# Performance work log

Hardware: AMD Instinct MI355X
Metric: run time of the kernel (lower is better)

Reference implementation:

```python
import jax, jax.numpy as jnp
import numpy as np

EPS = 1e-5

def _layernorm(x, g, b):
    mu = jnp.mean(x, axis=-1, keepdims=True)
    var = jnp.mean(jnp.square(x - mu), axis=-1, keepdims=True)
    return (x - mu) * jax.lax.rsqrt(var + EPS) * g + b

def _mlp(x, w1, b1, w2, b2):
    h = jax.nn.gelu(jnp.einsum('bnd,dh->bnh', x, w1) + b1, approximate=False)
    return jnp.einsum('bnh,hd->bnd', h, w2) + b2

def setup_inputs() -> dict:
    key = jax.random.key(0)
    B, N, D, H = 2, 8192, 1024, 4096
    ks = jax.random.split(key, 12)
    s1 = 1.0 / np.sqrt(D)
    s2 = 1.0 / np.sqrt(H)
    return {
        'x': jax.random.normal(ks[0], (B, N, D), dtype=jnp.float32),
        'mask': jax.random.randint(ks[1], (B, N), 0, 2) > 0,
        'g_rgb': jnp.ones((D,), jnp.float32),
        'b_rgb': jnp.zeros((D,), jnp.float32),
        'w1_rgb': jax.random.normal(ks[2], (D, H), dtype=jnp.float32) * s1,
        'b1_rgb': jnp.zeros((H,), jnp.float32),
        'w2_rgb': jax.random.normal(ks[3], (H, D), dtype=jnp.float32) * s2,
        'b2_rgb': jnp.zeros((D,), jnp.float32),
        'g_expr': jnp.ones((D,), jnp.float32),
        'b_expr': jnp.zeros((D,), jnp.float32),
        'w1_expr': jax.random.normal(ks[4], (D, H), dtype=jnp.float32) * s1,
        'b1_expr': jnp.zeros((H,), jnp.float32),
        'w2_expr': jax.random.normal(ks[5], (H, D), dtype=jnp.float32) * s2,
        'b2_expr': jnp.zeros((D,), jnp.float32),
    }

def reference(x, mask, g_rgb, b_rgb, w1_rgb, b1_rgb, w2_rgb, b2_rgb,
              g_expr, b_expr, w1_expr, b1_expr, w2_expr, b2_expr):
    # Per-token routing: rgb expert where mask, expr expert where ~mask.
    # LayerNorm+MLP are pointwise per token, so dense compute + select is
    # mathematically identical to the torch gather->compute->scatter.
    z_rgb = _mlp(_layernorm(x, g_rgb, b_rgb), w1_rgb, b1_rgb, w2_rgb, b2_rgb)
    z_expr = _mlp(_layernorm(x, g_expr, b_expr), w1_expr, b1_expr, w2_expr, b2_expr)
    z = jnp.where(mask[..., None], z_rgb, z_expr)
    return z.astype(jnp.float16)  # torch scatters into a float16 buffer
```

## Files before the change

kernel.cpp:

```cpp
#include <hip/hip_runtime.h>
#include <hip/hip_bf16.h>
#include <hip/hip_fp16.h>

#define D_ 1024
#define H_ 4096
#define NTOK 16384
#define MPAD 16640

typedef __attribute__((ext_vector_type(8))) short bf16x8;
typedef __attribute__((ext_vector_type(4))) float f32x4;

static __device__ __forceinline__ unsigned short f2bf(float f) {
  union { float f; unsigned u; } x; x.f = f;
  unsigned u = x.u + 0x7fffu + ((x.u >> 16) & 1u);
  return (unsigned short)(u >> 16);
}

static __device__ __forceinline__ void gld16(const void* g, void* l) {
  __builtin_amdgcn_global_load_lds(
      (const __attribute__((address_space(1))) unsigned int*)g,
      (__attribute__((address_space(3))) unsigned int*)l, 16, 0, 0);
}

static __device__ __forceinline__ float gelu_fast(float x) {
  const float z = x * (1.5957691216f + 0.0713548163f * x * x);
  return x * __builtin_amdgcn_rcpf(1.0f + __expf(-z));
}

__global__ __launch_bounds__(256) void transpose4_kernel(
    const float* __restrict__ w1r, const float* __restrict__ w1e,
    const float* __restrict__ w2r, const float* __restrict__ w2e,
    unsigned short* __restrict__ o1r, unsigned short* __restrict__ o1e,
    unsigned short* __restrict__ o2r, unsigned short* __restrict__ o2e,
    const int* __restrict__ mask, int* __restrict__ perm, int* __restrict__ counts) {
  __shared__ union SMem {
    float tile[64][65];
    struct { int sm[NTOK]; int wsum[4]; } c;
  } u;
  const int t = blockIdx.x;
  if (t == 4096) {
    const int NT = 256, CH = NTOK / NT;
    const int tt = threadIdx.x;
    const int ln = tt & 63, wv = tt >> 6;
    for (int i = tt; i < NTOK; i += NT) u.c.sm[i] = mask[i];
    for (int i = tt; i < MPAD; i += NT) perm[i] = -1;
    __syncthreads();
    const int base = tt * CH;
    int cnt = 0;
    for (int i = 0; i < CH; ++i) cnt += (u.c.sm[base + i] != 0);
    int sc = cnt;
#pragma unroll
    for (int o = 1; o < 64; o <<= 1) {
      int up = __shfl_up(sc, o, 64);
      if (ln >= o) sc += up;
    }
    if (ln == 63) u.c.wsum[wv] = sc;
    __syncthreads();
    int woff = 0;
#pragma unroll
    for (int j = 0; j < 4; ++j) woff += (j < wv) ? u.c.wsum[j] : 0;
    const int total1 = u.c.wsum[0] + u.c.wsum[1] + u.c.wsum[2] + u.c.wsum[3];
    if (tt == 0) { counts[0] = total1; counts[1] = NTOK - total1; }
    const int excl = woff + sc - cnt;
    const int expr_base = ((total1 + 255) >> 8) << 8;
    int p1 = excl;
    int p0 = expr_base + (base - excl);
    for (int i = 0; i < CH; ++i) {
      const int idx = base + i;
      if (u.c.sm[idx] != 0) perm[p1++] = idx; else perm[p0++] = idx;
    }
    return;
  }
  const float* src; unsigned short* dst; int R, C, tl;
  if (t < 1024)       { src = w1r; dst = o1r; R = D_; C = H_; tl = t; }
  else if (t < 2048)  { src = w1e; dst = o1e; R = D_; C = H_; tl = t - 1024; }
  else if (t < 3072)  { src = w2r; dst = o2r; R = H_; C = D_; tl = t - 2048; }
  else                { src = w2e; dst = o2e; R = H_; C = D_; tl = t - 3072; }
  const int tc = C >> 6;
  const int r0 = (tl / tc) * 64, c0 = (tl % tc) * 64;
  const int tx = threadIdx.x & 63, ty = threadIdx.x >> 6;
#pragma unroll
  for (int i = 0; i < 64; i += 4)
    u.tile[ty + i][tx] = src[(size_t)(r0 + ty + i) * C + c0 + tx];
  __syncthreads();
  const int wl = threadIdx.x & 31, wrow = threadIdx.x >> 5;
#pragma unroll
  for (int i = 0; i < 64; i += 8) {
    const int orow = wrow + i;
    const unsigned lo = f2bf(u.tile[2 * wl][orow]);
    const unsigned hi = f2bf(u.tile[2 * wl + 1][orow]);
    *(unsigned*)(dst + (size_t)(c0 + orow) * R + r0 + 2 * wl) = lo | (hi << 16);
  }
}

__global__ __launch_bounds__(512) void ln_kernel(
    const float* __restrict__ x, const int* __restrict__ mask,
    const int* __restrict__ perm,
    const float* __restrict__ g_rgb, const float* __restrict__ b_rgb,
    const float* __restrict__ g_expr, const float* __restrict__ b_expr,
    unsigned short* __restrict__ xln) {
  const int h = threadIdx.x >> 8;
  const int tid = threadIdx.x & 255;
  const int i = blockIdx.x * 2 + h;
  int t = perm[i];
  const bool live = t >= 0;
  if (!live) t = 0;
  const float4 v = ((const float4*)(x + (size_t)t * D_))[tid];
  float s = v.x + v.y + v.z + v.w;
  float ss = v.x * v.x + v.y * v.y + v.z * v.z + v.w * v.w;
#pragma unroll
  for (int o = 32; o > 0; o >>= 1) {
    s += __shfl_xor(s, o, 64);
    ss += __shfl_xor(ss, o, 64);
  }
  __shared__ float red[16];
  const int wv = threadIdx.x >> 6, ln = threadIdx.x & 63;
  if (ln == 0) { red[wv] = s; red[8 + wv] = ss; }
  __syncthreads();
  const int rb = h * 4;
  s = red[rb + 0] + red[rb + 1] + red[rb + 2] + red[rb + 3];
  ss = red[8 + rb + 0] + red[8 + rb + 1] + red[8 + rb + 2] + red[8 + rb + 3];
  const float mu = s * (1.0f / D_);
  const float var = ss * (1.0f / D_) - mu * mu;
  const float rs = rsqrtf(var + 1e-5f);
  const bool rgb = mask[t] != 0;
  const float4 gv = ((const float4*)(rgb ? g_rgb : g_expr))[tid];
  const float4 bv = ((const float4*)(rgb ? b_rgb : b_expr))[tid];
  const unsigned short o0 = f2bf((v.x - mu) * rs * gv.x + bv.x);
  const unsigned short o1 = f2bf((v.y - mu) * rs * gv.y + bv.y);
  const unsigned short o2 = f2bf((v.z - mu) * rs * gv.z + bv.z);
  const unsigned short o3 = f2bf((v.w - mu) * rs * gv.w + bv.w);
  uint2 pk;
  pk.x = (unsigned)o0 | ((unsigned)o1 << 16);
  pk.y = (unsigned)o2 | ((unsigned)o3 << 16);
  if (live) *((uint2*)(xln + (size_t)i * D_ + tid * 4)) = pk;
}

template <int K, int N>
__global__ __launch_bounds__(512, 2) void gemm8_kernel(
    const unsigned short* __restrict__ A,
    const unsigned short* __restrict__ Wt_rgb,
    const unsigned short* __restrict__ Wt_expr,
    const float* __restrict__ bias_rgb,
    const float* __restrict__ bias_expr,
    const int* __restrict__ counts,
    unsigned short* __restrict__ Out) {
  constexpr int MT = MPAD / 256;
  constexpr int NT = N / 256;
  constexpr int ntk = K / 64;
  constexpr int KH2 = 128 * K * 2;

  const int tid = threadIdx.x;
  const int id = blockIdx.x;
  const int xcd = id & 7;
  const int slot = id >> 3;
  const int p = xcd * ((MT * NT) / 8) + slot;
  const int m0 = (p / NT) * 256;
  const int n0 = (p % NT) * 256;
  const int cnt_rgb = counts[0];
  const unsigned short* Wt = (m0 < cnt_rgb) ? Wt_rgb : Wt_expr;
  const float* bias = (m0 < cnt_rgb) ? bias_rgb : bias_expr;

  __shared__ unsigned short As[2][256 * 64];
  __shared__ unsigned short Bs[2][256 * 64];

  const int lane = tid & 63, wave = tid >> 6;
  const int wr = wave >> 2, wc = wave & 3;
  const int quad = lane >> 4, l16 = lane & 15;

  f32x4 acc[8][4] = {};

  const char* Abase = (const char*)A;
  const char* Wbase = (const char*)Wt;

  int agK0, agK1, bgK0, bgK1, sl0, sl1;
  {
    const int s0 = tid, s1 = 512 + tid;
    const int r0 = s0 >> 3, r1 = s1 >> 3;
    const int ks0 = ((s0 ^ r0) & 7) * 8, ks1 = ((s1 ^ r1) & 7) * 8;
    agK0 = ((m0 + r0) * K + ks0) * 2;  agK1 = ((m0 + r1) * K + ks1) * 2;
    bgK0 = ((n0 + r0) * K + ks0) * 2;  bgK1 = ((n0 + r1) * K + ks1) * 2;
    sl0 = s0 * 16;  sl1 = s1 * 16;
  }

  int aoffL[2][2][4];
  int boffL[2][4];
#pragma unroll
  for (int kk = 0; kk < 2; ++kk) {
    const int cb = kk * 4 + quad;
#pragma unroll
    for (int mh = 0; mh < 2; ++mh)
#pragma unroll
      for (int mi = 0; mi < 4; ++mi) {
        const int row = wr * 128 + mh * 64 + mi * 16 + l16;
        aoffL[kk][mh][mi] = (row * 64 + ((cb ^ row) & 7) * 8) * 2;
      }
#pragma unroll
    for (int ni = 0; ni < 4; ++ni) {
      const int row = wc * 64 + ni * 16 + l16;
      boffL[kk][ni] = (row * 64 + ((cb ^ row) & 7) * 8) * 2;
    }
  }

  bf16x8 a0, a1, a2, a3;
  bf16x8 bb[4];

#define STAGE_A(T1, HA, Q) do { \
    gld16(Abase + agK0 + (HA) * KH2 + (T1) * 128, (char*)As + (Q) * 32768 + (HA) * 16384 + sl0); \
    gld16(Abase + agK1 + (HA) * KH2 + (T1) * 128, (char*)As + (Q) * 32768 + (HA) * 16384 + sl1); \
  } while (0)
#define STAGE_B(T2, HB, Q) do { \
    gld16(Wbase + bgK0 + (HB) * KH2 + (T2) * 128, (char*)Bs + (Q) * 32768 + (HB) * 16384 + sl0); \
    gld16(Wbase + bgK1 + (HB) * KH2 + (T2) * 128, (char*)Bs + (Q) * 32768 + (HB) * 16384 + sl1); \
  } while (0)
#define RD_A(P_, KK, MH) do { \
    const char* _ab = (const char*)As + (P_) * 32768; \
    a0 = *(const bf16x8*)(_ab + aoffL[KK][MH][0]); \
    a1 = *(const bf16x8*)(_ab + aoffL[KK][MH][1]); \
    a2 = *(const bf16x8*)(_ab + aoffL[KK][MH][2]); \
    a3 = *(const bf16x8*)(_ab + aoffL[KK][MH][3]); \
  } while (0)
#define RD_B(P_, KK) do { \
    const char* _bp = (const char*)Bs + (P_) * 32768; \
    bb[0] = *(const bf16x8*)(_bp + boffL[KK][0]); \
    bb[1] = *(const bf16x8*)(_bp + boffL[KK][1]); \
    bb[2] = *(const bf16x8*)(_bp + boffL[KK][2]); \
    bb[3] = *(const bf16x8*)(_bp + boffL[KK][3]); \
  } while (0)
#define MFMA16(MO) do { \
    acc[(MO)+0][0] = __builtin_amdgcn_mfma_f32_16x16x32_bf16(a0, bb[0], acc[(MO)+0][0], 0, 0, 0); \
    acc[(MO)+0][1] = __builtin_amdgcn_mfma_f32_16x16x32_bf16(a0, bb[1], acc[(MO)+0][1], 0, 0, 0); \
    acc[(MO)+0][2] = __builtin_amdgcn_mfma_f32_16x16x32_bf16(a0, bb[2], acc[(MO)+0][2], 0, 0, 0); \
    acc[(MO)+0][3] = __builtin_amdgcn_mfma_f32_16x16x32_bf16(a0, bb[3], acc[(MO)+0][3], 0, 0, 0); \
    acc[(MO)+1][0] = __builtin_amdgcn_mfma_f32_16x16x32_bf16(a1, bb[0], acc[(MO)+1][0], 0, 0, 0); \
    acc[(MO)+1][1] = __builtin_amdgcn_mfma_f32_16x16x32_bf16(a1, bb[1], acc[(MO)+1][1], 0, 0, 0); \
    acc[(MO)+1][2] = __builtin_amdgcn_mfma_f32_16x16x32_bf16(a1, bb[2], acc[(MO)+1][2], 0, 0, 0); \
    acc[(MO)+1][3] = __builtin_amdgcn_mfma_f32_16x16x32_bf16(a1, bb[3], acc[(MO)+1][3], 0, 0, 0); \
    acc[(MO)+2][0] = __builtin_amdgcn_mfma_f32_16x16x32_bf16(a2, bb[0], acc[(MO)+2][0], 0, 0, 0); \
    acc[(MO)+2][1] = __builtin_amdgcn_mfma_f32_16x16x32_bf16(a2, bb[1], acc[(MO)+2][1], 0, 0, 0); \
    acc[(MO)+2][2] = __builtin_amdgcn_mfma_f32_16x16x32_bf16(a2, bb[2], acc[(MO)+2][2], 0, 0, 0); \
    acc[(MO)+2][3] = __builtin_amdgcn_mfma_f32_16x16x32_bf16(a2, bb[3], acc[(MO)+2][3], 0, 0, 0); \
    acc[(MO)+3][0] = __builtin_amdgcn_mfma_f32_16x16x32_bf16(a3, bb[0], acc[(MO)+3][0], 0, 0, 0); \
    acc[(MO)+3][1] = __builtin_amdgcn_mfma_f32_16x16x32_bf16(a3, bb[1], acc[(MO)+3][1], 0, 0, 0); \
    acc[(MO)+3][2] = __builtin_amdgcn_mfma_f32_16x16x32_bf16(a3, bb[2], acc[(MO)+3][2], 0, 0, 0); \
    acc[(MO)+3][3] = __builtin_amdgcn_mfma_f32_16x16x32_bf16(a3, bb[3], acc[(MO)+3][3], 0, 0, 0); \
  } while (0)

#define KTILE(T_, P_, SA_, SB_, VMC_) do { \
     \
    RD_B(P_, 0); RD_A(P_, 0, 0); \
    if (SA_) STAGE_A((T_) + 1, 0, (P_) ^ 1); \
    __builtin_amdgcn_s_barrier(); \
    __builtin_amdgcn_s_setprio(1); MFMA16(0); __builtin_amdgcn_s_setprio(0); \
    __builtin_amdgcn_s_barrier(); \
     \
    RD_A(P_, 0, 1); \
    if (SA_) STAGE_A((T_) + 1, 1, (P_) ^ 1); \
    __builtin_amdgcn_s_barrier(); \
    __builtin_amdgcn_s_setprio(1); MFMA16(4); __builtin_amdgcn_s_setprio(0); \
    __builtin_amdgcn_s_barrier(); \
     \
    RD_B(P_, 1); RD_A(P_, 1, 0); \
    __builtin_amdgcn_s_barrier(); \
    __builtin_amdgcn_s_setprio(1); MFMA16(0); __builtin_amdgcn_s_setprio(0); \
    __builtin_amdgcn_s_barrier(); \
     \
    RD_A(P_, 1, 1); \
    if (SB_) { STAGE_B((T_) + 2, 0, P_); STAGE_B((T_) + 2, 1, P_); } \
    __builtin_amdgcn_s_barrier(); \
    __builtin_amdgcn_s_setprio(1); MFMA16(4); __builtin_amdgcn_s_setprio(0); \
    if ((VMC_) == 4) { asm volatile("s_waitcnt vmcnt(4)" ::: "memory"); } \
    else if ((VMC_) == 0) { asm volatile("s_waitcnt vmcnt(0)" ::: "memory"); } \
    __builtin_amdgcn_sched_barrier(0); \
    __builtin_amdgcn_s_barrier(); \
  } while (0)

  STAGE_A(0, 0, 0); STAGE_A(0, 1, 0);
  STAGE_B(0, 0, 0); STAGE_B(0, 1, 0);
  STAGE_B(1, 0, 1); STAGE_B(1, 1, 1);
  asm volatile("s_waitcnt vmcnt(4)" ::: "memory");
  __builtin_amdgcn_sched_barrier(0);
  __builtin_amdgcn_s_barrier();

  for (int tt = 0; tt < ntk / 2 - 1; ++tt) {
    const int t0 = tt * 2;
    KTILE(t0, 0, 1, 1, 4);
    KTILE(t0 + 1, 1, 1, 1, 4);
  }
  KTILE(ntk - 2, 0, 1, 0, 0);
  KTILE(ntk - 1, 1, 0, 0, -1);

#undef KTILE
#undef MFMA16
#undef RD_B
#undef RD_A
#undef STAGE_B
#undef STAGE_A

  float bv[4];
#pragma unroll
  for (int ni = 0; ni < 4; ++ni) bv[ni] = bias[n0 + wc * 64 + ni * 16 + l16];
#pragma unroll
  for (int mi = 0; mi < 8; ++mi) {
#pragma unroll
    for (int r = 0; r < 4; ++r) {
      const int row = m0 + wr * 128 + mi * 16 + quad * 4 + r;
      unsigned short* orow = Out + (size_t)row * N + n0 + wc * 64 + l16;
#pragma unroll
      for (int ni = 0; ni < 4; ++ni)
        orow[ni * 16] = f2bf(gelu_fast(acc[mi][ni][r] + bv[ni]));
    }
  }
}

template <int EP, int K, int N>
__global__ __launch_bounds__(256) void gemm_kernel(
    const unsigned short* __restrict__ A,
    const unsigned short* __restrict__ Wt_rgb,
    const unsigned short* __restrict__ Wt_expr,
    const float* __restrict__ bias_rgb,
    const float* __restrict__ bias_expr,
    const int* __restrict__ counts,
    const int* __restrict__ perm,
    void* __restrict__ OutP,
    const int mbase) {
  constexpr int BM = 128, BN = 128, BK = 64;
  constexpr int MTH = (MPAD / 2) / BM;
  constexpr int NT = N / BN;
  const int tid = threadIdx.x;
  const int id = blockIdx.x;
  const int xcd = id & 7;
  const int slot = id >> 3;
  const int p = xcd * ((MTH * NT) / 8) + slot;
  const int m0 = mbase + (p / NT) * BM;
  const int n0 = (p % NT) * BN;
  const int cnt_rgb = counts[0];
  const unsigned short* Wt = (m0 < cnt_rgb) ? Wt_rgb : Wt_expr;
  const float* bias = (m0 < cnt_rgb) ? bias_rgb : bias_expr;

  __shared__ unsigned short As[BM * BK];
  __shared__ unsigned short Bs[BN * BK];

  f32x4 acc[4][4] = {};

  const int lane = tid & 63, wave = tid >> 6;
  const int wm = (wave & 1) * 64, wn = (wave >> 1) * 64;
  const int quad = lane >> 4, l16 = lane & 15;

  const char* Abase = (const char*)A;
  const char* Wbase = (const char*)Wt;
  const char* AsB = (const char*)As;
  const char* BsB = (const char*)Bs;

  int ag[4], bg[4], sl[4];
#pragma unroll
  for (int it = 0; it < 4; ++it) {
    const int s = it * 256 + tid;
    const int row = s >> 3;
    const int ks = ((s ^ row) & 7) * 8;
    ag[it] = ((m0 + row) * K + ks) * 2;
    bg[it] = ((n0 + row) * K + ks) * 2;
    sl[it] = s * 16;
  }
  int aoff[2][4], boff[2][4];
#pragma unroll
  for (int hh = 0; hh < 2; ++hh) {
    const int cb = hh * 4 + quad;
#pragma unroll
    for (int mi = 0; mi < 4; ++mi) {
      const int row = wm + mi * 16 + l16;
      aoff[hh][mi] = (row * BK + (((cb ^ row) & 7) << 3)) * 2;
    }
#pragma unroll
    for (int ni = 0; ni < 4; ++ni) {
      const int row = wn + ni * 16 + l16;
      boff[hh][ni] = (row * BK + (((cb ^ row) & 7) << 3)) * 2;
    }
  }

  for (int k0 = 0; k0 < K; k0 += BK) {
#pragma unroll
    for (int it = 0; it < 4; ++it) {
      gld16(Abase + ag[it], (void*)(AsB + sl[it]));
      gld16(Wbase + bg[it], (void*)(BsB + sl[it]));
      ag[it] += BK * 2;
      bg[it] += BK * 2;
    }
    __syncthreads();
#pragma unroll
    for (int hh = 0; hh < 2; ++hh) {
      bf16x8 a[4], b[4];
#pragma unroll
      for (int mi = 0; mi < 4; ++mi) a[mi] = *(const bf16x8*)(AsB + aoff[hh][mi]);
#pragma unroll
      for (int ni = 0; ni < 4; ++ni) b[ni] = *(const bf16x8*)(BsB + boff[hh][ni]);
#pragma unroll
      for (int mi = 0; mi < 4; ++mi)
#pragma unroll
        for (int ni = 0; ni < 4; ++ni)
          acc[mi][ni] = __builtin_amdgcn_mfma_f32_16x16x32_bf16(a[mi], b[ni], acc[mi][ni], 0, 0, 0);
    }
    __syncthreads();
  }

  float bv[4];
#pragma unroll
  for (int ni = 0; ni < 4; ++ni) bv[ni] = bias[n0 + wn + ni * 16 + l16];

#pragma unroll
  for (int mi = 0; mi < 4; ++mi) {
#pragma unroll
    for (int r = 0; r < 4; ++r) {
      const int row = m0 + wm + mi * 16 + quad * 4 + r;
      if (EP == 0) {
        unsigned short* orow = (unsigned short*)OutP + (size_t)row * N + n0 + wn + l16;
#pragma unroll
        for (int ni = 0; ni < 4; ++ni) {
          orow[ni * 16] = f2bf(gelu_fast(acc[mi][ni][r] + bv[ni]));
        }
      } else {
        const int p2 = perm[row];
        if (p2 < 0) continue;
        float* orow = (float*)OutP + (size_t)p2 * N + n0 + wn + l16;
#pragma unroll
        for (int ni = 0; ni < 4; ++ni) {
          float v = acc[mi][ni][r] + bv[ni];
          orow[ni * 16] = __half2float(__float2half_rn(v));
        }
      }
    }
  }
}

extern "C" void kernel_launch(void* const* d_in, const int* in_sizes, int n_in,
                              void* d_out, int out_size, void* d_ws, size_t ws_size,
                              hipStream_t stream) {
  const float* x       = (const float*)d_in[0];
  const int*   mask    = (const int*)d_in[1];
  const float* g_rgb   = (const float*)d_in[2];
  const float* b_rgb   = (const float*)d_in[3];
  const float* w1_rgb  = (const float*)d_in[4];
  const float* b1_rgb  = (const float*)d_in[5];
  const float* w2_rgb  = (const float*)d_in[6];
  const float* b2_rgb  = (const float*)d_in[7];
  const float* g_expr  = (const float*)d_in[8];
  const float* b_expr  = (const float*)d_in[9];
  const float* w1_expr = (const float*)d_in[10];
  const float* b1_expr = (const float*)d_in[11];
  const float* w2_expr = (const float*)d_in[12];
  const float* b2_expr = (const float*)d_in[13];

  char* w = (char*)d_ws;
  int* counts               = (int*)(w + 0);
  int* perm                 = (int*)(w + 256);
  unsigned short* w1t_rgb   = (unsigned short*)(w + 66816);
  unsigned short* w1t_expr  = (unsigned short*)(w + 8455424);
  unsigned short* w2t_rgb   = (unsigned short*)(w + 16844032);
  unsigned short* w2t_expr  = (unsigned short*)(w + 25232640);
  unsigned short* xln       = (unsigned short*)(w + 33621248);
  unsigned short* h         = (unsigned short*)(w + 67699968);

  transpose4_kernel<<<4097, 256, 0, stream>>>(
      w1_rgb, w1_expr, w2_rgb, w2_expr, w1t_rgb, w1t_expr, w2t_rgb, w2t_expr,
      mask, perm, counts);

  ln_kernel<<<MPAD / 2, 512, 0, stream>>>(x, mask, perm, g_rgb, b_rgb, g_expr, b_expr, xln);

  gemm8_kernel<D_, H_><<<dim3((MPAD / 256) * (H_ / 256)), 512, 0, stream>>>(
      xln, w1t_rgb, w1t_expr, b1_rgb, b1_expr, counts, h);

  gemm_kernel<1, H_, D_><<<dim3((D_ / 128) * (MPAD / 2 / 128)), 256, 0, stream>>>(
      h, w2t_rgb, w2t_expr, b2_rgb, b2_expr, counts, perm, d_out, 0);
  gemm_kernel<1, H_, D_><<<dim3((D_ / 128) * (MPAD / 2 / 128)), 256, 0, stream>>>(
      h, w2t_rgb, w2t_expr, b2_rgb, b2_expr, counts, perm, d_out, MPAD / 2);
}
```

Baseline: 591.3 us.

## Replace barrier-interleaved K-loop with simple double buffer and register prefetch

```diff
diff --git a/kernel.cpp b/kernel.cpp
--- a/kernel.cpp
+++ b/kernel.cpp
@@ -202,8 +202,8 @@
     }
   }
 
-  bf16x8 a0, a1, a2, a3;
-  bf16x8 bb[4];
+  bf16x8 aX0, aX1, aX2, aX3, aY0, aY1, aY2, aY3;
+  bf16x8 b00, b01, b02, b03, b10, b11, b12, b13;
 
 #define STAGE_A(T1, HA, Q) do { \
     gld16(Abase + agK0 + (HA) * KH2 + (T1) * 128, (char*)As + (Q) * 32768 + (HA) * 16384 + sl0); \
@@ -213,87 +213,76 @@
     gld16(Wbase + bgK0 + (HB) * KH2 + (T2) * 128, (char*)Bs + (Q) * 32768 + (HB) * 16384 + sl0); \
     gld16(Wbase + bgK1 + (HB) * KH2 + (T2) * 128, (char*)Bs + (Q) * 32768 + (HB) * 16384 + sl1); \
   } while (0)
-#define RD_A(P_, KK, MH) do { \
+#define RD_A4(D0, D1, D2, D3, P_, KK, MH) do { \
     const char* _ab = (const char*)As + (P_) * 32768; \
-    a0 = *(const bf16x8*)(_ab + aoffL[KK][MH][0]); \
-    a1 = *(const bf16x8*)(_ab + aoffL[KK][MH][1]); \
-    a2 = *(const bf16x8*)(_ab + aoffL[KK][MH][2]); \
-    a3 = *(const bf16x8*)(_ab + aoffL[KK][MH][3]); \
-  } while (0)
-#define RD_B(P_, KK) do { \
+    D0 = *(const bf16x8*)(_ab + aoffL[KK][MH][0]); \
+    D1 = *(const bf16x8*)(_ab + aoffL[KK][MH][1]); \
+    D2 = *(const bf16x8*)(_ab + aoffL[KK][MH][2]); \
+    D3 = *(const bf16x8*)(_ab + aoffL[KK][MH][3]); \
+  } while (0)
+#define RD_B4(D0, D1, D2, D3, P_, KK) do { \
     const char* _bp = (const char*)Bs + (P_) * 32768; \
-    bb[0] = *(const bf16x8*)(_bp + boffL[KK][0]); \
-    bb[1] = *(const bf16x8*)(_bp + boffL[KK][1]); \
-    bb[2] = *(const bf16x8*)(_bp + boffL[KK][2]); \
-    bb[3] = *(const bf16x8*)(_bp + boffL[KK][3]); \
-  } while (0)
-#define MFMA16(MO) do { \
-    acc[(MO)+0][0] = __builtin_amdgcn_mfma_f32_16x16x32_bf16(a0, bb[0], acc[(MO)+0][0], 0, 0, 0); \
-    acc[(MO)+0][1] = __builtin_amdgcn_mfma_f32_16x16x32_bf16(a0, bb[1], acc[(MO)+0][1], 0, 0, 0); \
-    acc[(MO)+0][2] = __builtin_amdgcn_mfma_f32_16x16x32_bf16(a0, bb[2], acc[(MO)+0][2], 0, 0, 0); \
-    acc[(MO)+0][3] = __builtin_amdgcn_mfma_f32_16x16x32_bf16(a0, bb[3], acc[(MO)+0][3], 0, 0, 0); \
-    acc[(MO)+1][0] = __builtin_amdgcn_mfma_f32_16x16x32_bf16(a1, bb[0], acc[(MO)+1][0], 0, 0, 0); \
-    acc[(MO)+1][1] = __builtin_amdgcn_mfma_f32_16x16x32_bf16(a1, bb[1], acc[(MO)+1][1], 0, 0, 0); \
-    acc[(MO)+1][2] = __builtin_amdgcn_mfma_f32_16x16x32_bf16(a1, bb[2], acc[(MO)+1][2], 0, 0, 0); \
-    acc[(MO)+1][3] = __builtin_amdgcn_mfma_f32_16x16x32_bf16(a1, bb[3], acc[(MO)+1][3], 0, 0, 0); \
-    acc[(MO)+2][0] = __builtin_amdgcn_mfma_f32_16x16x32_bf16(a2, bb[0], acc[(MO)+2][0], 0, 0, 0); \
-    acc[(MO)+2][1] = __builtin_amdgcn_mfma_f32_16x16x32_bf16(a2, bb[1], acc[(MO)+2][1], 0, 0, 0); \
-    acc[(MO)+2][2] = __builtin_amdgcn_mfma_f32_16x16x32_bf16(a2, bb[2], acc[(MO)+2][2], 0, 0, 0); \
-    acc[(MO)+2][3] = __builtin_amdgcn_mfma_f32_16x16x32_bf16(a2, bb[3], acc[(MO)+2][3], 0, 0, 0); \
-    acc[(MO)+3][0] = __builtin_amdgcn_mfma_f32_16x16x32_bf16(a3, bb[0], acc[(MO)+3][0], 0, 0, 0); \
-    acc[(MO)+3][1] = __builtin_amdgcn_mfma_f32_16x16x32_bf16(a3, bb[1], acc[(MO)+3][1], 0, 0, 0); \
-    acc[(MO)+3][2] = __builtin_amdgcn_mfma_f32_16x16x32_bf16(a3, bb[2], acc[(MO)+3][2], 0, 0, 0); \
-    acc[(MO)+3][3] = __builtin_amdgcn_mfma_f32_16x16x32_bf16(a3, bb[3], acc[(MO)+3][3], 0, 0, 0); \
-  } while (0)
-
-#define KTILE(T_, P_, SA_, SB_, VMC_) do { \
-     \
-    RD_B(P_, 0); RD_A(P_, 0, 0); \
-    if (SA_) STAGE_A((T_) + 1, 0, (P_) ^ 1); \
-    __builtin_amdgcn_s_barrier(); \
-    __builtin_amdgcn_s_setprio(1); MFMA16(0); __builtin_amdgcn_s_setprio(0); \
-    __builtin_amdgcn_s_barrier(); \
-     \
-    RD_A(P_, 0, 1); \
-    if (SA_) STAGE_A((T_) + 1, 1, (P_) ^ 1); \
-    __builtin_amdgcn_s_barrier(); \
-    __builtin_amdgcn_s_setprio(1); MFMA16(4); __builtin_amdgcn_s_setprio(0); \
-    __builtin_amdgcn_s_barrier(); \
-     \
-    RD_B(P_, 1); RD_A(P_, 1, 0); \
-    __builtin_amdgcn_s_barrier(); \
-    __builtin_amdgcn_s_setprio(1); MFMA16(0); __builtin_amdgcn_s_setprio(0); \
-    __builtin_amdgcn_s_barrier(); \
-     \
-    RD_A(P_, 1, 1); \
-    if (SB_) { STAGE_B((T_) + 2, 0, P_); STAGE_B((T_) + 2, 1, P_); } \
-    __builtin_amdgcn_s_barrier(); \
-    __builtin_amdgcn_s_setprio(1); MFMA16(4); __builtin_amdgcn_s_setprio(0); \
-    if ((VMC_) == 4) { asm volatile("s_waitcnt vmcnt(4)" ::: "memory"); } \
-    else if ((VMC_) == 0) { asm volatile("s_waitcnt vmcnt(0)" ::: "memory"); } \
-    __builtin_amdgcn_sched_barrier(0); \
-    __builtin_amdgcn_s_barrier(); \
+    D0 = *(const bf16x8*)(_bp + boffL[KK][0]); \
+    D1 = *(const bf16x8*)(_bp + boffL[KK][1]); \
+    D2 = *(const bf16x8*)(_bp + boffL[KK][2]); \
+    D3 = *(const bf16x8*)(_bp + boffL[KK][3]); \
+  } while (0)
+#define MFMA16(A0_, A1_, A2_, A3_, B0_, B1_, B2_, B3_, MO) do { \
+    acc[(MO)+0][0] = __builtin_amdgcn_mfma_f32_16x16x32_bf16(A0_, B0_, acc[(MO)+0][0], 0, 0, 0); \
+    acc[(MO)+0][1] = __builtin_amdgcn_mfma_f32_16x16x32_bf16(A0_, B1_, acc[(MO)+0][1], 0, 0, 0); \
+    acc[(MO)+0][2] = __builtin_amdgcn_mfma_f32_16x16x32_bf16(A0_, B2_, acc[(MO)+0][2], 0, 0, 0); \
+    acc[(MO)+0][3] = __builtin_amdgcn_mfma_f32_16x16x32_bf16(A0_, B3_, acc[(MO)+0][3], 0, 0, 0); \
+    acc[(MO)+1][0] = __builtin_amdgcn_mfma_f32_16x16x32_bf16(A1_, B0_, acc[(MO)+1][0], 0, 0, 0); \
+    acc[(MO)+1][1] = __builtin_amdgcn_mfma_f32_16x16x32_bf16(A1_, B1_, acc[(MO)+1][1], 0, 0, 0); \
+    acc[(MO)+1][2] = __builtin_amdgcn_mfma_f32_16x16x32_bf16(A1_, B2_, acc[(MO)+1][2], 0, 0, 0); \
+    acc[(MO)+1][3] = __builtin_amdgcn_mfma_f32_16x16x32_bf16(A1_, B3_, acc[(MO)+1][3], 0, 0, 0); \
+    acc[(MO)+2][0] = __builtin_amdgcn_mfma_f32_16x16x32_bf16(A2_, B0_, acc[(MO)+2][0], 0, 0, 0); \
+    acc[(MO)+2][1] = __builtin_amdgcn_mfma_f32_16x16x32_bf16(A2_, B1_, acc[(MO)+2][1], 0, 0, 0); \
+    acc[(MO)+2][2] = __builtin_amdgcn_mfma_f32_16x16x32_bf16(A2_, B2_, acc[(MO)+2][2], 0, 0, 0); \
+    acc[(MO)+2][3] = __builtin_amdgcn_mfma_f32_16x16x32_bf16(A2_, B3_, acc[(MO)+2][3], 0, 0, 0); \
+    acc[(MO)+3][0] = __builtin_amdgcn_mfma_f32_16x16x32_bf16(A3_, B0_, acc[(MO)+3][0], 0, 0, 0); \
+    acc[(MO)+3][1] = __builtin_amdgcn_mfma_f32_16x16x32_bf16(A3_, B1_, acc[(MO)+3][1], 0, 0, 0); \
+    acc[(MO)+3][2] = __builtin_amdgcn_mfma_f32_16x16x32_bf16(A3_, B2_, acc[(MO)+3][2], 0, 0, 0); \
+    acc[(MO)+3][3] = __builtin_amdgcn_mfma_f32_16x16x32_bf16(A3_, B3_, acc[(MO)+3][3], 0, 0, 0); \
+  } while (0)
+
+#define KTILE(P_, T1_, ST_) do { \
+    if (ST_) { \
+      STAGE_A(T1_, 0, (P_) ^ 1); STAGE_A(T1_, 1, (P_) ^ 1); \
+      STAGE_B(T1_, 0, (P_) ^ 1); STAGE_B(T1_, 1, (P_) ^ 1); \
+    } \
+    RD_B4(b00, b01, b02, b03, P_, 0); \
+    RD_A4(aX0, aX1, aX2, aX3, P_, 0, 0); \
+    RD_A4(aY0, aY1, aY2, aY3, P_, 0, 1); \
+    RD_B4(b10, b11, b12, b13, P_, 1); \
+    __builtin_amdgcn_s_setprio(1); \
+    MFMA16(aX0, aX1, aX2, aX3, b00, b01, b02, b03, 0); \
+    __builtin_amdgcn_s_setprio(0); \
+    RD_A4(aX0, aX1, aX2, aX3, P_, 1, 0); \
+    __builtin_amdgcn_s_setprio(1); \
+    MFMA16(aY0, aY1, aY2, aY3, b00, b01, b02, b03, 4); \
+    __builtin_amdgcn_s_setprio(0); \
+    RD_A4(aY0, aY1, aY2, aY3, P_, 1, 1); \
+    __builtin_amdgcn_s_setprio(1); \
+    MFMA16(aX0, aX1, aX2, aX3, b10, b11, b12, b13, 0); \
+    MFMA16(aY0, aY1, aY2, aY3, b10, b11, b12, b13, 4); \
+    __builtin_amdgcn_s_setprio(0); \
+    __syncthreads(); \
   } while (0)
 
   STAGE_A(0, 0, 0); STAGE_A(0, 1, 0);
   STAGE_B(0, 0, 0); STAGE_B(0, 1, 0);
-  STAGE_B(1, 0, 1); STAGE_B(1, 1, 1);
-  asm volatile("s_waitcnt vmcnt(4)" ::: "memory");
-  __builtin_amdgcn_sched_barrier(0);
-  __builtin_amdgcn_s_barrier();
-
-  for (int tt = 0; tt < ntk / 2 - 1; ++tt) {
-    const int t0 = tt * 2;
-    KTILE(t0, 0, 1, 1, 4);
-    KTILE(t0 + 1, 1, 1, 1, 4);
-  }
-  KTILE(ntk - 2, 0, 1, 0, 0);
-  KTILE(ntk - 1, 1, 0, 0, -1);
+  __syncthreads();
+
+  for (int tt = 0; tt < ntk / 2; ++tt) {
+    KTILE(0, 2 * tt + 1, 1);
+    KTILE(1, 2 * tt + 2, tt < ntk / 2 - 1);
+  }
 
 #undef KTILE
 #undef MFMA16
-#undef RD_B
-#undef RD_A
+#undef RD_B4
+#undef RD_A4
 #undef STAGE_B
 #undef STAGE_A
 
```

Measured after the change: 587.9 us. Within noise of the previous version (-0.6%).
